# Kernel optimization log

Hardware: AMD Instinct MI355X
Metric: run time of the kernel (lower is better)

## Reference

```python
import jax, jax.numpy as jnp
import numpy as np
from functools import partial

B, T, D = 4, 1024, 1024
NH = 16            # n_branches
DH = D // NH       # d_branch = 64
SOMA_H = int(D * 3.0)
EPS = 1e-5

def _gelu(x):
    return jax.nn.gelu(x, approximate=False)  # torch default GELU is exact erf

def _gconv(x_cf, w, b, pad_left, groups):
    # x_cf: [B, C_in, T], w: [C_out, C_in//groups, K] (torch OIW layout)
    y = jax.lax.conv_general_dilated(
        x_cf, w, window_strides=(1,), padding=[(pad_left, 0)],
        feature_group_count=groups, dimension_numbers=('NCH', 'OIH', 'NCH'))
    return y + b[None, :, None]

def setup_inputs() -> dict:
    key = jax.random.key(0)
    ks = jax.random.split(key, 16)
    s = 0.02
    return {
        'x': jax.random.normal(ks[0], (B, T, D), jnp.float32),
        'nmda': jax.random.normal(ks[1], (B, NH, DH), jnp.float32),
        'qkv_w': jax.random.normal(ks[2], (D, 3 * D), jnp.float32) * s,
        'nmda_decay': jax.random.normal(ks[3], (1, NH, 1, DH), jnp.float32) * 0.1 + 0.9,
        'tconv_w': jax.random.normal(ks[4], (D, DH, 5), jnp.float32) * s,
        'tconv_b': jnp.zeros((D,), jnp.float32),
        'ffu_w': jax.random.normal(ks[5], (2 * D, DH, 1), jnp.float32) * s,
        'ffu_b': jnp.zeros((2 * D,), jnp.float32),
        'ffd_w': jax.random.normal(ks[6], (D, 2 * DH, 1), jnp.float32) * s,
        'ffd_b': jnp.zeros((D,), jnp.float32),
        'gn_w': jnp.ones((D,), jnp.float32),
        'gn_b': jnp.zeros((D,), jnp.float32),
        'soma_w': jax.random.normal(ks[7], (D, D), jnp.float32) * s,
        'ln_w': jnp.ones((D,), jnp.float32),
        'ln_b': jnp.zeros((D,), jnp.float32),
        'w1': jax.random.normal(ks[8], (D, SOMA_H), jnp.float32) * s,
        'b1': jnp.zeros((SOMA_H,), jnp.float32),
        'w2': jax.random.normal(ks[9], (SOMA_H, D), jnp.float32) * s,
        'b2': jnp.zeros((D,), jnp.float32),
    }

def reference(x, nmda, qkv_w, nmda_decay, tconv_w, tconv_b, ffu_w, ffu_b,
              ffd_w, ffd_b, gn_w, gn_b, soma_w, ln_w, ln_b, w1, b1, w2, b2):
    # QKV projection -> [B, T, 3, NH, DH] -> Q,K,V [B, NH, T, DH]
    qkv = (x @ qkv_w).reshape(B, T, 3, NH, DH).transpose(2, 0, 3, 1, 4)
    Q, K, V = qkv[0], qkv[1], qkv[2]
    # NMDA trace injection into V, gated by sigmoid(decay)
    tau = jax.nn.sigmoid(nmda_decay)                    # [1, NH, 1, DH]
    V = V + nmda[:, :, None, :] * tau
    # causal SDPA
    scale = 1.0 / jnp.sqrt(jnp.asarray(DH, x.dtype))
    scores = jnp.einsum('bhqd,bhkd->bhqk', Q, K) * scale
    causal = jnp.tril(jnp.ones((T, T), bool))
    scores = jnp.where(causal[None, None], scores, jnp.finfo(x.dtype).min)
    attn = jnp.einsum('bhqk,bhkd->bhqd', jax.nn.softmax(scores, axis=-1), V)
    branch_flat = attn.transpose(0, 2, 1, 3).reshape(B, T, D)   # [B,T,D]
    # causal temporal grouped conv (pad=4, k=5, truncated to T => left-pad 4)
    x_cf = branch_flat.transpose(0, 2, 1)                       # [B,D,T]
    x_cf = x_cf + _gconv(x_cf, tconv_w, tconv_b, 4, NH)
    # grouped 1x1 FFN
    ff_hidden = _gelu(_gconv(x_cf, ffu_w, ffu_b, 0, NH))        # [B,2D,T]
    ff_out = _gconv(ff_hidden, ffd_w, ffd_b, 0, NH).transpose(0, 2, 1)
    residual = branch_flat + ff_out
    # GroupNorm over each branch's DH channels (per token)
    r = residual.reshape(B, T, NH, DH)
    mu = r.mean(-1, keepdims=True)
    var = ((r - mu) ** 2).mean(-1, keepdims=True)
    normed_heads = (r - mu) / jnp.sqrt(var + EPS)
    normed_heads = normed_heads * gn_w.reshape(NH, DH) + gn_b.reshape(NH, DH)
    normed = normed_heads.reshape(B, T, D)
    # NMDA state update from last token
    branch_last = normed_heads[:, -1]                           # [B,NH,DH]
    tau2 = jax.nn.sigmoid(nmda_decay[:, :, 0, :])               # [1,NH,DH]
    new_nmda = tau2 * nmda + (1.0 - tau2) * branch_last
    # soma projection + LN + FFN (exact GELU)
    soma = normed @ soma_w
    mu2 = soma.mean(-1, keepdims=True)
    var2 = ((soma - mu2) ** 2).mean(-1, keepdims=True)
    lns = (soma - mu2) / jnp.sqrt(var2 + EPS) * ln_w + ln_b
    soma = soma + (_gelu(lns @ w1 + b1) @ w2 + b2)
    return soma, new_nmda
```

## Files before the change

kernel.cpp:

```cpp
#include <hip/hip_runtime.h>
#include <math.h>

#define B_  4
#define T_  1024
#define D_  1024
#define NH_ 16
#define DH_ 64
#define SH_ 3072

typedef unsigned short u16;
typedef __attribute__((ext_vector_type(8))) short bf16x8;
typedef __attribute__((ext_vector_type(4))) float f32x4;
typedef __attribute__((ext_vector_type(4))) unsigned short u16x4;
typedef __attribute__((ext_vector_type(8))) unsigned short u16x8;

__device__ __forceinline__ float gelu_f(float x) {
    return 0.5f * x * (1.0f + erff(x * 0.70710678118654752440f));
}
__device__ __forceinline__ float sigm_f(float x) {
    return 1.0f / (1.0f + __expf(-x));
}
__device__ __forceinline__ u16 f2bf(float f) {
    unsigned u = __builtin_bit_cast(unsigned, f);
    return (u16)((u + 0x7FFFu + ((u >> 16) & 1u)) >> 16);
}

#define GLD16(gsrc, ldst) __builtin_amdgcn_global_load_lds( \
    (__attribute__((address_space(1))) void*)(gsrc),        \
    (__attribute__((address_space(3))) void*)(ldst), 16, 0, 0)

__global__ __launch_bounds__(256) void cast_bf16_k(
    const float* __restrict__ in, u16* __restrict__ out, int n8)
{
    int i = blockIdx.x * 256 + threadIdx.x;
    if (i >= n8) return;
    const float4* p = (const float4*)(in + (size_t)i * 8);
    float4 a = p[0], b = p[1];
    u16x8 o;
    o[0] = f2bf(a.x); o[1] = f2bf(a.y); o[2] = f2bf(a.z); o[3] = f2bf(a.w);
    o[4] = f2bf(b.x); o[5] = f2bf(b.y); o[6] = f2bf(b.z); o[7] = f2bf(b.w);
    *(u16x8*)(out + (size_t)i * 8) = o;
}

__global__ __launch_bounds__(256) void transpose_cast_k(
    const float* __restrict__ W, u16* __restrict__ Wt, int K, int N)
{
    __shared__ float t[32][33];
    const int n0 = blockIdx.x * 32, k0 = blockIdx.y * 32;
    const int tid = threadIdx.x;
    {
        int kr = tid >> 3, nc = (tid & 7) * 4;
        float4 v = *(const float4*)(W + (size_t)(k0 + kr) * N + n0 + nc);
        t[kr][nc] = v.x; t[kr][nc + 1] = v.y; t[kr][nc + 2] = v.z; t[kr][nc + 3] = v.w;
    }
    __syncthreads();
    {
        int nr = tid >> 3, kc = (tid & 7) * 4;
        u16x4 o = { f2bf(t[kc][nr]), f2bf(t[kc + 1][nr]),
                    f2bf(t[kc + 2][nr]), f2bf(t[kc + 3][nr]) };
        *(u16x4*)(Wt + (size_t)(n0 + nr) * K + k0 + kc) = o;
    }
}

__global__ __launch_bounds__(256) void tconv_wprep(
    const float* __restrict__ w, u16* __restrict__ Wtp)
{
    int idx = blockIdx.x * 256 + threadIdx.x;
    int c = idx / 320, r = idx - c * 320;
    int k5 = r >> 6, i = r & 63;
    Wtp[idx] = f2bf(w[c * 320 + i * 5 + k5]);
}

template<bool BIAS, bool GELU, bool ACCUM, bool BF16OUT>
__global__ __launch_bounds__(256) void gemm_mfma(
    const u16* __restrict__ A, const u16* __restrict__ Bt,
    const float* __restrict__ bias, void* __restrict__ Cv,
    int M, int N, int K)
{
    __shared__ u16 As[4096];
    __shared__ u16 Bs[4096];
    const int tid = threadIdx.x;
    const int m0 = blockIdx.y * 128, n0 = blockIdx.x * 128;
    const int w = tid >> 6, l = tid & 63;
    const int mw = (w >> 1) * 64, nw = (w & 1) * 64;
    const int lr = l & 15, kg = l >> 4;
    const int swz = kg ^ ((lr >> 1) & 3);

    f32x4 acc[4][4];
#pragma unroll
    for (int i = 0; i < 4; ++i)
#pragma unroll
        for (int j = 0; j < 4; ++j) acc[i][j] = (f32x4){0.f, 0.f, 0.f, 0.f};

    const int mA0 = tid >> 2;
    const int kg0 = (tid & 3) ^ ((mA0 >> 1) & 3);
    const int mA1 = (256 + tid) >> 2;
    const int kg1 = ((256 + tid) & 3) ^ ((mA1 >> 1) & 3);
    const u16* a0 = A + (size_t)(m0 + mA0) * K + kg0 * 8;
    const u16* a1 = A + (size_t)(m0 + mA1) * K + kg1 * 8;
    const u16* b0 = Bt + (size_t)(n0 + mA0) * K + kg0 * 8;
    const u16* b1 = Bt + (size_t)(n0 + mA1) * K + kg1 * 8;
    u16* lA0 = As + tid * 8;  u16* lA1 = As + (256 + tid) * 8;
    u16* lB0 = Bs + tid * 8;  u16* lB1 = Bs + (256 + tid) * 8;

    for (int k0 = 0; k0 < K; k0 += 32) {
        __syncthreads();
        GLD16(a0 + k0, lA0); GLD16(a1 + k0, lA1);
        GLD16(b0 + k0, lB0); GLD16(b1 + k0, lB1);
        __syncthreads();

        bf16x8 aF[4], bF[4];
#pragma unroll
        for (int mt = 0; mt < 4; ++mt) {
            int row = mw + mt * 16 + lr;
            aF[mt] = *(const bf16x8*)&As[(row * 4 + swz) * 8];
            int rowb = nw + mt * 16 + lr;
            bF[mt] = *(const bf16x8*)&Bs[(rowb * 4 + swz) * 8];
        }
#pragma unroll
        for (int mt = 0; mt < 4; ++mt)
#pragma unroll
            for (int nt = 0; nt < 4; ++nt)
                acc[mt][nt] = __builtin_amdgcn_mfma_f32_16x16x32_bf16(
                    aF[mt], bF[nt], acc[mt][nt], 0, 0, 0);
    }

    const int lq = l >> 4;
#pragma unroll
    for (int mt = 0; mt < 4; ++mt) {
#pragma unroll
        for (int nt = 0; nt < 4; ++nt) {
            int row = m0 + mw + mt * 16 + lq * 4;
            int col = n0 + nw + nt * 16 + lr;
            float bsv = BIAS ? bias[col] : 0.f;
#pragma unroll
            for (int j = 0; j < 4; ++j) {
                float v = acc[mt][nt][j] + bsv;
                if (GELU) v = gelu_f(v);
                size_t idx = (size_t)(row + j) * N + col;
                if (BF16OUT) {
                    ((u16*)Cv)[idx] = f2bf(v);
                } else {
                    float* C = (float*)Cv;
                    if (ACCUM) v += C[idx];
                    C[idx] = v;
                }
            }
        }
    }
}

__global__ __launch_bounds__(256) void attn_mfma(
    const u16* __restrict__ qkv, const float* __restrict__ nmda,
    const float* __restrict__ nmda_decay, float* __restrict__ branch)
{
    const int qt = 15 - (int)blockIdx.x;
    const int h  = blockIdx.y;
    const int b  = blockIdx.z;
    const int tid = threadIdx.x;
    const int w  = tid >> 6, l = tid & 63;
    const int lr = l & 15, kg = l >> 4;
    const int q0 = qt * 64;

    __shared__ u16 Ks[64 * 64];
    __shared__ u16 Vrow[64 * 64];
    __shared__ u16 Vt[64 * 64];
    __shared__ u16 Ps[4][16 * 64];

    bf16x8 qf[2];
    {
        const u16* qrow = qkv + (size_t)(b * T_ + q0 + w * 16 + lr) * (3 * D_) + h * 64;
        qf[0] = *(const bf16x8*)(qrow + kg * 8);
        qf[1] = *(const bf16x8*)(qrow + 32 + kg * 8);
    }

    float nshift[4];
#pragma unroll
    for (int nt = 0; nt < 4; ++nt) {
        int d = nt * 16 + lr;
        nshift[nt] = nmda[(size_t)(b * NH_ + h) * 64 + d] * sigm_f(nmda_decay[h * 64 + d]);
    }

    f32x4 O[4];
#pragma unroll
    for (int nt = 0; nt < 4; ++nt) O[nt] = (f32x4){0.f, 0.f, 0.f, 0.f};
    float m_run[4] = {-INFINITY, -INFINITY, -INFINITY, -INFINITY};
    float l_run[4] = {0.f, 0.f, 0.f, 0.f};

    const int p0 = tid, p1 = 256 + tid;
    const int kr0 = p0 >> 3, ks0 = p0 & 7;
    const int kr1 = p1 >> 3, ks1 = p1 & 7;
    const u16* kbase = qkv + (size_t)(b * T_) * (3 * D_) + D_ + h * 64;
    const u16* vbase = kbase + D_;
    const u16* ksrc0 = kbase + (size_t)kr0 * (3 * D_) + ((ks0 ^ (kr0 & 7)) << 3);
    const u16* ksrc1 = kbase + (size_t)kr1 * (3 * D_) + ((ks1 ^ (kr1 & 7)) << 3);
    const u16* vsrc0 = vbase + (size_t)kr0 * (3 * D_) + (ks0 << 3);
    const u16* vsrc1 = vbase + (size_t)kr1 * (3 * D_) + (ks1 << 3);

    for (int kt = 0; kt <= qt; ++kt) {
        const size_t off = (size_t)(kt * 64) * (3 * D_);
        __syncthreads();
        GLD16(ksrc0 + off, Ks + p0 * 8);
        GLD16(ksrc1 + off, Ks + p1 * 8);
        GLD16(vsrc0 + off, Vrow + p0 * 8);
        GLD16(vsrc1 + off, Vrow + p1 * 8);
        __syncthreads();

        {
            const int d = l;
#pragma unroll
            for (int pp = 0; pp < 2; ++pp) {
                const int gk = w + pp * 4;
                u16x8 col;
#pragma unroll
                for (int j = 0; j < 8; ++j)
                    col[j] = Vrow[(gk * 8 + j) * 64 + d];
                *(u16x8*)&Vt[d * 64 + ((gk ^ (d & 7)) << 3)] = col;
            }
        }

        f32x4 s[4];
#pragma unroll
        for (int nt = 0; nt < 4; ++nt) s[nt] = (f32x4){0.f, 0.f, 0.f, 0.f};
#pragma unroll
        for (int ks = 0; ks < 2; ++ks) {
#pragma unroll
            for (int nt = 0; nt < 4; ++nt) {
                int krow = nt * 16 + lr;
                bf16x8 kf = *(const bf16x8*)&Ks[krow * 64 + (((ks * 4 + kg) ^ (krow & 7)) << 3)];
                s[nt] = __builtin_amdgcn_mfma_f32_16x16x32_bf16(qf[ks], kf, s[nt], 0, 0, 0);
            }
        }
#pragma unroll
        for (int nt = 0; nt < 4; ++nt)
#pragma unroll
            for (int j = 0; j < 4; ++j) s[nt][j] *= 0.125f;

        __syncthreads();

        if (kt == qt) {
#pragma unroll
            for (int nt = 0; nt < 4; ++nt) {
                int kvp = nt * 16 + lr;
#pragma unroll
                for (int j = 0; j < 4; ++j) {
                    int qp = w * 16 + kg * 4 + j;
                    if (kvp > qp) s[nt][j] = -INFINITY;
                }
            }
        }

        float c4[4];
#pragma unroll
        for (int j = 0; j < 4; ++j) {
            float mx = fmaxf(fmaxf(s[0][j], s[1][j]), fmaxf(s[2][j], s[3][j]));
#pragma unroll
            for (int msk = 1; msk < 16; msk <<= 1) mx = fmaxf(mx, __shfl_xor(mx, msk));
            float mn = fmaxf(m_run[j], mx);
            c4[j] = __expf(m_run[j] - mn);
            m_run[j] = mn;
            float ls = 0.f;
#pragma unroll
            for (int nt = 0; nt < 4; ++nt) {
                float p = __expf(s[nt][j] - mn);
                s[nt][j] = p;
                ls += p;
            }
#pragma unroll
            for (int msk = 1; msk < 16; msk <<= 1) ls += __shfl_xor(ls, msk);
            l_run[j] = l_run[j] * c4[j] + ls;
        }

#pragma unroll
        for (int nt = 0; nt < 4; ++nt) {
#pragma unroll
            for (int j = 0; j < 4; ++j) {
                int r = kg * 4 + j;
                int c = nt * 16 + lr;
                Ps[w][r * 64 + (((c >> 3) ^ (r & 7)) << 3) + (c & 7)] = f2bf(s[nt][j]);
            }
        }

#pragma unroll
        for (int nt = 0; nt < 4; ++nt)
#pragma unroll
            for (int j = 0; j < 4; ++j) O[nt][j] *= c4[j];
#pragma unroll
        for (int ks = 0; ks < 2; ++ks) {
            bf16x8 pa = *(const bf16x8*)&Ps[w][lr * 64 + (((ks * 4 + kg) ^ (lr & 7)) << 3)];
#pragma unroll
            for (int nt = 0; nt < 4; ++nt) {
                int vrow = nt * 16 + lr;
                bf16x8 vf = *(const bf16x8*)&Vt[vrow * 64 + (((ks * 4 + kg) ^ (vrow & 7)) << 3)];
                O[nt] = __builtin_amdgcn_mfma_f32_16x16x32_bf16(pa, vf, O[nt], 0, 0, 0);
            }
        }
    }

#pragma unroll
    for (int j = 0; j < 4; ++j) {
        float inv = 1.f / l_run[j];
        int qrow = q0 + w * 16 + kg * 4 + j;
        float* orow = branch + (size_t)(b * T_ + qrow) * D_ + h * 64;
#pragma unroll
        for (int nt = 0; nt < 4; ++nt)
            orow[nt * 16 + lr] = O[nt][j] * inv + nshift[nt];
    }
}

__global__ __launch_bounds__(256) void tconv_mfma(
    const float* __restrict__ branch, const u16* __restrict__ Wtp,
    const float* __restrict__ bias, float* __restrict__ xcf2)
{
    const int tid = threadIdx.x;
    const int t0 = blockIdx.x * 128;
    const int g  = blockIdx.y;
    const int b  = blockIdx.z;
    const int w = tid >> 6, l = tid & 63;
    const int lr = l & 15, kg = l >> 4;
    const int mw = (w >> 1) * 64;
    const int nw = (w & 1) * 32;

    __shared__ u16 xbf[132 * 64];
    __shared__ u16 Bs[64 * 32];

    for (int idx = tid; idx < 132 * 8; idx += 256) {
        int row = idx >> 3, gr = idx & 7;
        int tg = t0 - 4 + row;
        u16x8 v8 = (u16x8){0, 0, 0, 0, 0, 0, 0, 0};
        if (tg >= 0) {
            const float* src = &branch[(size_t)(b * T_ + tg) * D_ + g * 64 + gr * 8];
            float4 f0 = *(const float4*)src;
            float4 f1 = *(const float4*)(src + 4);
            v8[0] = f2bf(f0.x); v8[1] = f2bf(f0.y); v8[2] = f2bf(f0.z); v8[3] = f2bf(f0.w);
            v8[4] = f2bf(f1.x); v8[5] = f2bf(f1.y); v8[6] = f2bf(f1.z); v8[7] = f2bf(f1.w);
        }
        *(u16x8*)&xbf[row * 64 + ((gr ^ (row & 7)) << 3)] = v8;
    }

    f32x4 acc[4][2];
#pragma unroll
    for (int i = 0; i < 4; ++i)
#pragma unroll
        for (int j = 0; j < 2; ++j) acc[i][j] = (f32x4){0.f, 0.f, 0.f, 0.f};

    const int mB  = tid >> 2;
    const int kgb = (tid & 3) ^ ((mB >> 1) & 3);
    const u16* bsrc = Wtp + (size_t)(g * 64 + mB) * 320 + kgb * 8;
    u16* lB = Bs + tid * 8;
    const int swzB = kg ^ ((lr >> 1) & 3);

    for (int k0 = 0; k0 < 320; k0 += 32) {
        __syncthreads();
        GLD16(bsrc + k0, lB);
        __syncthreads();

        const int kgr = (k0 >> 3) + kg;
        const int k5  = kgr >> 3;
        const int ig  = kgr & 7;

        bf16x8 aF[4];
#pragma unroll
        for (int mt = 0; mt < 4; ++mt) {
            int row = mw + mt * 16 + lr + k5;
            aF[mt] = *(const bf16x8*)&xbf[row * 64 + ((ig ^ (row & 7)) << 3)];
        }
        bf16x8 bF[2];
#pragma unroll
        for (int nt = 0; nt < 2; ++nt) {
            int rb = nw + nt * 16 + lr;
            bF[nt] = *(const bf16x8*)&Bs[(rb * 4 + swzB) * 8];
        }
#pragma unroll
        for (int mt = 0; mt < 4; ++mt)
#pragma unroll
            for (int nt = 0; nt < 2; ++nt)
                acc[mt][nt] = __builtin_amdgcn_mfma_f32_16x16x32_bf16(
                    aF[mt], bF[nt], acc[mt][nt], 0, 0, 0);
    }

    const int lq = l >> 4;
#pragma unroll
    for (int mt = 0; mt < 4; ++mt) {
#pragma unroll
        for (int nt = 0; nt < 2; ++nt) {
            int trow = t0 + mw + mt * 16 + lq * 4;
            int col  = g * 64 + nw + nt * 16 + lr;
            float bv = bias[col];
#pragma unroll
            for (int j = 0; j < 4; ++j) {
                size_t idx = (size_t)(b * T_ + trow + j) * D_ + col;
                xcf2[idx] = acc[mt][nt][j] + bv + branch[idx];
            }
        }
    }
}

__global__ __launch_bounds__(256) void ffu_kernel(
    const float* __restrict__ xcf2, const float* __restrict__ w,
    const float* __restrict__ bias, float* __restrict__ hid)
{
    const int tid = threadIdx.x;
    const int t0 = blockIdx.x * 64, g = blockIdx.y, b = blockIdx.z;
    __shared__ __align__(16) float al[64][68];
    __shared__ __align__(16) float wlds[64][132];

    for (int idx = tid; idx < 64 * 64; idx += 256) {
        int i = idx & 63, tl = idx >> 6;
        al[i][tl] = xcf2[(size_t)(b * T_ + t0 + tl) * D_ + g * 64 + i];
    }
    for (int idx = tid; idx < 128 * 64; idx += 256) {
        int i = idx & 63, o = idx >> 6;
        wlds[i][o] = w[(size_t)(g * 128 + o) * 64 + i];
    }
    __syncthreads();

    const int ot = (tid & 15) * 8;
    const int tt = (tid >> 4) * 4;
    float acc[4][8];
#pragma unroll
    for (int i = 0; i < 4; ++i)
#pragma unroll
        for (int j = 0; j < 8; ++j) acc[i][j] = 0.f;

#pragma unroll 8
    for (int i = 0; i < 64; ++i) {
        float4 a4 = *(const float4*)&al[i][tt];
        float4 w0 = *(const float4*)&wlds[i][ot];
        float4 w1 = *(const float4*)&wlds[i][ot + 4];
        float av[4] = {a4.x, a4.y, a4.z, a4.w};
        float wv[8] = {w0.x, w0.y, w0.z, w0.w, w1.x, w1.y, w1.z, w1.w};
#pragma unroll
        for (int ti = 0; ti < 4; ++ti)
#pragma unroll
            for (int oi = 0; oi < 8; ++oi)
                acc[ti][oi] = fmaf(av[ti], wv[oi], acc[ti][oi]);
    }

    float4 bb0 = *(const float4*)&bias[g * 128 + ot];
    float4 bb1 = *(const float4*)&bias[g * 128 + ot + 4];
    float bv[8] = {bb0.x, bb0.y, bb0.z, bb0.w, bb1.x, bb1.y, bb1.z, bb1.w};
#pragma unroll
    for (int ti = 0; ti < 4; ++ti) {
        float o_[8];
#pragma unroll
        for (int oi = 0; oi < 8; ++oi) o_[oi] = gelu_f(acc[ti][oi] + bv[oi]);
        float* hp = hid + (size_t)(b * T_ + t0 + tt + ti) * (2 * D_) + g * 128 + ot;
        *(float4*)hp       = make_float4(o_[0], o_[1], o_[2], o_[3]);
        *(float4*)(hp + 4) = make_float4(o_[4], o_[5], o_[6], o_[7]);
    }
}

__global__ __launch_bounds__(256) void ffd_gn_kernel(
    const float* __restrict__ hid, const float* __restrict__ w,
    const float* __restrict__ bias, const float* __restrict__ branch,
    const float* __restrict__ gn_w, const float* __restrict__ gn_b,
    const float* __restrict__ nmda, const float* __restrict__ nmda_decay,
    u16* __restrict__ normed, float* __restrict__ out_nmda)
{
    const int tid = threadIdx.x;
    const int t0 = blockIdx.x * 32, g = blockIdx.y, b = blockIdx.z;
    __shared__ __align__(16) float al[128][36];
    __shared__ __align__(16) float wl[128][68];

    for (int idx = tid; idx < 128 * 32; idx += 256) {
        int j = idx & 127, tl = idx >> 7;
        al[j][tl] = hid[(size_t)(b * T_ + t0 + tl) * (2 * D_) + g * 128 + j];
    }
    for (int idx = tid; idx < 64 * 128; idx += 256) {
        int j = idx & 127, c = idx >> 7;
        wl[j][c] = w[(size_t)(g * 64 + c) * 128 + j];
    }
    __syncthreads();

    const int c0 = (tid & 15) * 4;
    const int tt = (tid >> 4) * 2;
    float acc[2][4];
#pragma unroll
    for (int i = 0; i < 2; ++i)
#pragma unroll
        for (int j = 0; j < 4; ++j) acc[i][j] = 0.f;

#pragma unroll 8
    for (int j = 0; j < 128; ++j) {
        float2 a2 = *(const float2*)&al[j][tt];
        float4 w4 = *(const float4*)&wl[j][c0];
        acc[0][0] = fmaf(a2.x, w4.x, acc[0][0]);
        acc[0][1] = fmaf(a2.x, w4.y, acc[0][1]);
        acc[0][2] = fmaf(a2.x, w4.z, acc[0][2]);
        acc[0][3] = fmaf(a2.x, w4.w, acc[0][3]);
        acc[1][0] = fmaf(a2.y, w4.x, acc[1][0]);
        acc[1][1] = fmaf(a2.y, w4.y, acc[1][1]);
        acc[1][2] = fmaf(a2.y, w4.z, acc[1][2]);
        acc[1][3] = fmaf(a2.y, w4.w, acc[1][3]);
    }

    float4 bb = *(const float4*)&bias[g * 64 + c0];
    float4 gw = *(const float4*)&gn_w[g * 64 + c0];
    float4 gb = *(const float4*)&gn_b[g * 64 + c0];

#pragma unroll
    for (int tq = 0; tq < 2; ++tq) {
        const int tg = t0 + tt + tq;
        float4 br = *(const float4*)&branch[(size_t)(b * T_ + tg) * D_ + g * 64 + c0];
        float r0 = br.x + acc[tq][0] + bb.x;
        float r1 = br.y + acc[tq][1] + bb.y;
        float r2 = br.z + acc[tq][2] + bb.z;
        float r3 = br.w + acc[tq][3] + bb.w;
        float sm = r0 + r1 + r2 + r3;
#pragma unroll
        for (int m = 1; m < 16; m <<= 1) sm += __shfl_xor(sm, m);
        float mu = sm * (1.f / 64.f);
        float d0 = r0 - mu, d1 = r1 - mu, d2 = r2 - mu, d3 = r3 - mu;
        float vs = d0 * d0 + d1 * d1 + d2 * d2 + d3 * d3;
#pragma unroll
        for (int m = 1; m < 16; m <<= 1) vs += __shfl_xor(vs, m);
        float is = rsqrtf(vs * (1.f / 64.f) + 1e-5f);
        float n0 = d0 * is * gw.x + gb.x;
        float n1 = d1 * is * gw.y + gb.y;
        float n2 = d2 * is * gw.z + gb.z;
        float n3 = d3 * is * gw.w + gb.w;
        u16x4 o = { f2bf(n0), f2bf(n1), f2bf(n2), f2bf(n3) };
        *(u16x4*)&normed[(size_t)(b * T_ + tg) * D_ + g * 64 + c0] = o;
        if (tg == T_ - 1) {
            float nv[4] = {n0, n1, n2, n3};
#pragma unroll
            for (int cc = 0; cc < 4; ++cc) {
                int dloc = c0 + cc;
                int ni = (b * NH_ + g) * 64 + dloc;
                float t2 = sigm_f(nmda_decay[g * 64 + dloc]);
                out_nmda[ni] = t2 * nmda[ni] + (1.f - t2) * nv[cc];
            }
        }
    }
}

__global__ __launch_bounds__(256) void ln_kernel(
    const float* __restrict__ x, const float* __restrict__ w,
    const float* __restrict__ bo, u16* __restrict__ y)
{
    __shared__ float red[8];
    const int row = blockIdx.x, tid = threadIdx.x;
    const float* xr = x + (size_t)row * D_;
    float4 v = *(const float4*)&xr[tid * 4];
    float s = v.x + v.y + v.z + v.w;
#pragma unroll
    for (int m = 32; m; m >>= 1) s += __shfl_xor(s, m);
    if ((tid & 63) == 0) red[tid >> 6] = s;
    __syncthreads();
    float mu = (red[0] + red[1] + red[2] + red[3]) * (1.f / 1024.f);
    float dx = v.x - mu, dy = v.y - mu, dz = v.z - mu, dw = v.w - mu;
    float q = dx * dx + dy * dy + dz * dz + dw * dw;
#pragma unroll
    for (int m = 32; m; m >>= 1) q += __shfl_xor(q, m);
    if ((tid & 63) == 0) red[4 + (tid >> 6)] = q;
    __syncthreads();
    float var = (red[4] + red[5] + red[6] + red[7]) * (1.f / 1024.f);
    float is = rsqrtf(var + 1e-5f);
    float4 wv = *(const float4*)&w[tid * 4];
    float4 bv = *(const float4*)&bo[tid * 4];
    u16x4 o = { f2bf(dx * is * wv.x + bv.x), f2bf(dy * is * wv.y + bv.y),
                f2bf(dz * is * wv.z + bv.z), f2bf(dw * is * wv.w + bv.w) };
    *(u16x4*)&y[(size_t)row * D_ + tid * 4] = o;
}

extern "C" void kernel_launch(void* const* d_in, const int* in_sizes, int n_in,
                              void* d_out, int out_size, void* d_ws, size_t ws_size,
                              hipStream_t stream)
{
    const float* x       = (const float*)d_in[0];
    const float* nmda    = (const float*)d_in[1];
    const float* qkv_w   = (const float*)d_in[2];
    const float* nmda_d  = (const float*)d_in[3];
    const float* tconv_w = (const float*)d_in[4];
    const float* tconv_b = (const float*)d_in[5];
    const float* ffu_w   = (const float*)d_in[6];
    const float* ffu_b   = (const float*)d_in[7];
    const float* ffd_w   = (const float*)d_in[8];
    const float* ffd_b   = (const float*)d_in[9];
    const float* gn_w    = (const float*)d_in[10];
    const float* gn_b    = (const float*)d_in[11];
    const float* soma_w  = (const float*)d_in[12];
    const float* ln_w    = (const float*)d_in[13];
    const float* ln_b    = (const float*)d_in[14];
    const float* w1      = (const float*)d_in[15];
    const float* b1      = (const float*)d_in[16];
    const float* w2      = (const float*)d_in[17];
    const float* b2      = (const float*)d_in[18];
    (void)in_sizes; (void)n_in; (void)out_size; (void)ws_size;

    float* outp     = (float*)d_out;
    float* soma     = outp;
    float* out_nmda = outp + (size_t)B_ * T_ * D_;

    float* ws     = (float*)d_ws;
    float* branch = ws;
    float* xcf2   = ws + (size_t)4194304;
    float* normed = ws + (size_t)8388608;
    float* qkvb   = ws + (size_t)12582912;
    u16*   qkvbf = (u16*)qkvb;
    float* hid   = qkvb;
    u16*   h1bf  = (u16*)qkvb;

    u16* xbf    = (u16*)normed;
    u16* wqkvT  = (u16*)normed + 4194304;
    u16* Wtp    = (u16*)normed + 7340032;
    u16* normbf = (u16*)xcf2;
    u16* somaT  = (u16*)xcf2 + 4194304;
    u16* lnsbf  = (u16*)branch;
    u16* w1T    = (u16*)branch + 4194304;
    u16* w2T    = (u16*)xcf2;

    hipLaunchKernelGGL(tconv_wprep, dim3(1280), dim3(256), 0, stream, tconv_w, Wtp);
    hipLaunchKernelGGL(cast_bf16_k, dim3(2048), dim3(256), 0, stream, x, xbf, 524288);
    hipLaunchKernelGGL(transpose_cast_k, dim3(96, 32), dim3(256), 0, stream,
                       qkv_w, wqkvT, 1024, 3072);
    hipLaunchKernelGGL((gemm_mfma<false, false, false, true>), dim3(24, 32), dim3(256), 0, stream,
                       xbf, wqkvT, nullptr, qkvbf, 4096, 3072, 1024);
    hipLaunchKernelGGL(attn_mfma, dim3(16, NH_, B_), dim3(256), 0, stream,
                       qkvbf, nmda, nmda_d, branch);
    hipLaunchKernelGGL(tconv_mfma, dim3(8, NH_, B_), dim3(256), 0, stream,
                       branch, Wtp, tconv_b, xcf2);
    hipLaunchKernelGGL(ffu_kernel, dim3(16, NH_, B_), dim3(256), 0, stream,
                       xcf2, ffu_w, ffu_b, hid);
    hipLaunchKernelGGL(ffd_gn_kernel, dim3(32, NH_, B_), dim3(256), 0, stream,
                       hid, ffd_w, ffd_b, branch, gn_w, gn_b, nmda, nmda_d,
                       normbf, out_nmda);
    hipLaunchKernelGGL(transpose_cast_k, dim3(32, 32), dim3(256), 0, stream,
                       soma_w, somaT, 1024, 1024);
    hipLaunchKernelGGL((gemm_mfma<false, false, false, false>), dim3(8, 32), dim3(256), 0, stream,
                       normbf, somaT, nullptr, soma, 4096, 1024, 1024);
    hipLaunchKernelGGL(ln_kernel, dim3(B_ * T_), dim3(256), 0, stream,
                       soma, ln_w, ln_b, lnsbf);
    hipLaunchKernelGGL(transpose_cast_k, dim3(96, 32), dim3(256), 0, stream,
                       w1, w1T, 1024, 3072);
    hipLaunchKernelGGL((gemm_mfma<true, true, false, true>), dim3(24, 32), dim3(256), 0, stream,
                       lnsbf, w1T, b1, h1bf, 4096, 3072, 1024);
    hipLaunchKernelGGL(transpose_cast_k, dim3(32, 96), dim3(256), 0, stream,
                       w2, w2T, 3072, 1024);
    hipLaunchKernelGGL((gemm_mfma<true, false, true, false>), dim3(8, 32), dim3(256), 0, stream,
                       h1bf, w2T, b2, soma, 4096, 1024, 3072);
}
```

Before: 489.7 us.

## Deepen GEMM K-tile to 64 and narrow N-tile for N=1024 GEMMs

The MFMA GEMM now stages 64-wide K slices per barrier pair instead of 32, with a new 8-way XOR swizzle for the wider LDS rows, which halves the number of synchronisation rounds. A template parameter sets the N tile width, and the two N=1024 GEMMs switch to 128x64 tiles so they launch twice as many workgroups and fill more compute units. The cost is more LDS per block and, for the narrow tiles, less reuse of the A tile.

```diff
diff --git a/kernel.cpp b/kernel.cpp
--- a/kernel.cpp
+++ b/kernel.cpp
@@ -71,65 +71,78 @@
     Wtp[idx] = f2bf(w[c * 320 + i * 5 + k5]);
 }
 
-template<bool BIAS, bool GELU, bool ACCUM, bool BF16OUT>
+template<int NF, bool BIAS, bool GELU, bool ACCUM, bool BF16OUT>
 __global__ __launch_bounds__(256) void gemm_mfma(
     const u16* __restrict__ A, const u16* __restrict__ Bt,
     const float* __restrict__ bias, void* __restrict__ Cv,
     int M, int N, int K)
 {
-    __shared__ u16 As[4096];
-    __shared__ u16 Bs[4096];
+    constexpr int BN = 32 * NF;
+    __shared__ u16 As[128 * 64];
+    __shared__ u16 Bs[BN * 64];
     const int tid = threadIdx.x;
-    const int m0 = blockIdx.y * 128, n0 = blockIdx.x * 128;
+    const int m0 = blockIdx.y * 128, n0 = blockIdx.x * BN;
     const int w = tid >> 6, l = tid & 63;
-    const int mw = (w >> 1) * 64, nw = (w & 1) * 64;
+    const int mw = (w >> 1) * 64, nw = (w & 1) * (NF * 16);
     const int lr = l & 15, kg = l >> 4;
-    const int swz = kg ^ ((lr >> 1) & 3);
-
-    f32x4 acc[4][4];
+
+    f32x4 acc[4][NF];
 #pragma unroll
     for (int i = 0; i < 4; ++i)
 #pragma unroll
-        for (int j = 0; j < 4; ++j) acc[i][j] = (f32x4){0.f, 0.f, 0.f, 0.f};
-
-    const int mA0 = tid >> 2;
-    const int kg0 = (tid & 3) ^ ((mA0 >> 1) & 3);
-    const int mA1 = (256 + tid) >> 2;
-    const int kg1 = ((256 + tid) & 3) ^ ((mA1 >> 1) & 3);
-    const u16* a0 = A + (size_t)(m0 + mA0) * K + kg0 * 8;
-    const u16* a1 = A + (size_t)(m0 + mA1) * K + kg1 * 8;
-    const u16* b0 = Bt + (size_t)(n0 + mA0) * K + kg0 * 8;
-    const u16* b1 = Bt + (size_t)(n0 + mA1) * K + kg1 * 8;
-    u16* lA0 = As + tid * 8;  u16* lA1 = As + (256 + tid) * 8;
-    u16* lB0 = Bs + tid * 8;  u16* lB1 = Bs + (256 + tid) * 8;
-
-    for (int k0 = 0; k0 < K; k0 += 32) {
+        for (int j = 0; j < NF; ++j) acc[i][j] = (f32x4){0.f, 0.f, 0.f, 0.f};
+
+    const u16* aSrc[4]; u16* lA[4];
+#pragma unroll
+    for (int i = 0; i < 4; ++i) {
+        int p = i * 256 + tid, row = p >> 3, sg = (p & 7) ^ (row & 7);
+        aSrc[i] = A + (size_t)(m0 + row) * K + sg * 8;
+        lA[i] = As + p * 8;
+    }
+    const u16* bSrc[NF]; u16* lB[NF];
+#pragma unroll
+    for (int i = 0; i < NF; ++i) {
+        int p = i * 256 + tid, row = p >> 3, sg = (p & 7) ^ (row & 7);
+        bSrc[i] = Bt + (size_t)(n0 + row) * K + sg * 8;
+        lB[i] = Bs + p * 8;
+    }
+
+    for (int k0 = 0; k0 < K; k0 += 64) {
         __syncthreads();
-        GLD16(a0 + k0, lA0); GLD16(a1 + k0, lA1);
-        GLD16(b0 + k0, lB0); GLD16(b1 + k0, lB1);
+#pragma unroll
+        for (int i = 0; i < 4; ++i) GLD16(aSrc[i] + k0, lA[i]);
+#pragma unroll
+        for (int i = 0; i < NF; ++i) GLD16(bSrc[i] + k0, lB[i]);
         __syncthreads();
 
-        bf16x8 aF[4], bF[4];
-#pragma unroll
-        for (int mt = 0; mt < 4; ++mt) {
-            int row = mw + mt * 16 + lr;
-            aF[mt] = *(const bf16x8*)&As[(row * 4 + swz) * 8];
-            int rowb = nw + mt * 16 + lr;
-            bF[mt] = *(const bf16x8*)&Bs[(rowb * 4 + swz) * 8];
-        }
-#pragma unroll
-        for (int mt = 0; mt < 4; ++mt)
-#pragma unroll
-            for (int nt = 0; nt < 4; ++nt)
-                acc[mt][nt] = __builtin_amdgcn_mfma_f32_16x16x32_bf16(
-                    aF[mt], bF[nt], acc[mt][nt], 0, 0, 0);
+#pragma unroll
+        for (int ks = 0; ks < 2; ++ks) {
+            const int g = ks * 4 + kg;
+            bf16x8 aF[4], bF[NF];
+#pragma unroll
+            for (int mt = 0; mt < 4; ++mt) {
+                int row = mw + mt * 16 + lr;
+                aF[mt] = *(const bf16x8*)&As[row * 64 + ((g ^ (row & 7)) << 3)];
+            }
+#pragma unroll
+            for (int nt = 0; nt < NF; ++nt) {
+                int rb = nw + nt * 16 + lr;
+                bF[nt] = *(const bf16x8*)&Bs[rb * 64 + ((g ^ (rb & 7)) << 3)];
+            }
+#pragma unroll
+            for (int mt = 0; mt < 4; ++mt)
+#pragma unroll
+                for (int nt = 0; nt < NF; ++nt)
+                    acc[mt][nt] = __builtin_amdgcn_mfma_f32_16x16x32_bf16(
+                        aF[mt], bF[nt], acc[mt][nt], 0, 0, 0);
+        }
     }
 
     const int lq = l >> 4;
 #pragma unroll
     for (int mt = 0; mt < 4; ++mt) {
 #pragma unroll
-        for (int nt = 0; nt < 4; ++nt) {
+        for (int nt = 0; nt < NF; ++nt) {
             int row = m0 + mw + mt * 16 + lq * 4;
             int col = n0 + nw + nt * 16 + lr;
             float bsv = BIAS ? bias[col] : 0.f;
@@ -615,7 +628,7 @@
     hipLaunchKernelGGL(cast_bf16_k, dim3(2048), dim3(256), 0, stream, x, xbf, 524288);
     hipLaunchKernelGGL(transpose_cast_k, dim3(96, 32), dim3(256), 0, stream,
                        qkv_w, wqkvT, 1024, 3072);
-    hipLaunchKernelGGL((gemm_mfma<false, false, false, true>), dim3(24, 32), dim3(256), 0, stream,
+    hipLaunchKernelGGL((gemm_mfma<4, false, false, false, true>), dim3(24, 32), dim3(256), 0, stream,
                        xbf, wqkvT, nullptr, qkvbf, 4096, 3072, 1024);
     hipLaunchKernelGGL(attn_mfma, dim3(16, NH_, B_), dim3(256), 0, stream,
                        qkvbf, nmda, nmda_d, branch);
@@ -628,16 +641,16 @@
                        normbf, out_nmda);
     hipLaunchKernelGGL(transpose_cast_k, dim3(32, 32), dim3(256), 0, stream,
                        soma_w, somaT, 1024, 1024);
-    hipLaunchKernelGGL((gemm_mfma<false, false, false, false>), dim3(8, 32), dim3(256), 0, stream,
+    hipLaunchKernelGGL((gemm_mfma<2, false, false, false, false>), dim3(16, 32), dim3(256), 0, stream,
                        normbf, somaT, nullptr, soma, 4096, 1024, 1024);
     hipLaunchKernelGGL(ln_kernel, dim3(B_ * T_), dim3(256), 0, stream,
                        soma, ln_w, ln_b, lnsbf);
     hipLaunchKernelGGL(transpose_cast_k, dim3(96, 32), dim3(256), 0, stream,
                        w1, w1T, 1024, 3072);
-    hipLaunchKernelGGL((gemm_mfma<true, true, false, true>), dim3(24, 32), dim3(256), 0, stream,
+    hipLaunchKernelGGL((gemm_mfma<4, true, true, false, true>), dim3(24, 32), dim3(256), 0, stream,
                        lnsbf, w1T, b1, h1bf, 4096, 3072, 1024);
     hipLaunchKernelGGL(transpose_cast_k, dim3(32, 96), dim3(256), 0, stream,
                        w2, w2T, 3072, 1024);
-    hipLaunchKernelGGL((gemm_mfma<true, false, true, false>), dim3(8, 32), dim3(256), 0, stream,
+    hipLaunchKernelGGL((gemm_mfma<2, true, false, true, false>), dim3(16, 32), dim3(256), 0, stream,
                        h1bf, w2T, b2, soma, 4096, 1024, 3072);
 }
```

After: 441.3 us. 9.9% less time.
